# Performance work log

Hardware: AMD Instinct MI355X
Metric: run time of the kernel (lower is better)

## Reference

```python
import jax, jax.numpy as jnp
import numpy as np

DIM = 768
HEADS = 8
EPS = 1e-6


def _layernorm(x, gamma, beta):
    # torch: mean over last dim; std with Bessel correction (unbiased, ddof=1)
    mean = jnp.mean(x, axis=-1, keepdims=True)
    std = jnp.std(x, axis=-1, keepdims=True, ddof=1)
    return gamma * (x - mean) / (std + EPS) + beta


def setup_inputs() -> dict:
    key = jax.random.key(0)
    ks = jax.random.split(key, 8)
    s = 0.02
    return {
        "x": jax.random.normal(ks[0], (16384, DIM), dtype=jnp.float32),
        "wq_w": jax.random.normal(ks[1], (DIM, DIM), dtype=jnp.float32) * s,
        "wq_b": jnp.zeros((DIM,), dtype=jnp.float32),
        "wk_w": jax.random.normal(ks[2], (DIM, DIM), dtype=jnp.float32) * s,
        "wk_b": jnp.zeros((DIM,), dtype=jnp.float32),
        "wv_w": jax.random.normal(ks[3], (DIM, DIM), dtype=jnp.float32) * s,
        "wv_b": jnp.zeros((DIM,), dtype=jnp.float32),
        "d1_w": jax.random.normal(ks[4], (4 * DIM, DIM), dtype=jnp.float32) * s,
        "d1_b": jnp.zeros((4 * DIM,), dtype=jnp.float32),
        "d2_w": jax.random.normal(ks[5], (DIM, 4 * DIM), dtype=jnp.float32) * s,
        "d2_b": jnp.zeros((DIM,), dtype=jnp.float32),
        "g1": jnp.ones((1,), dtype=jnp.float32),
        "b1": jnp.zeros((1,), dtype=jnp.float32),
        "g2": jnp.ones((1,), dtype=jnp.float32),
        "b2": jnp.zeros((1,), dtype=jnp.float32),
    }


def reference(x, wq_w, wq_b, wk_w, wk_b, wv_w, wv_b,
              d1_w, d1_b, d2_w, d2_b, g1, b1, g2, b2):
    T = x.shape[0]
    # --- pre-LN + attention ---
    xn = _layernorm(x, g1, b1)                      # [T, D]
    q = xn @ wq_w.T + wq_b                          # [T, D]
    k = xn @ wk_w.T + wk_b
    v = xn @ wv_w.T + wv_b
    # faithful to q.view(-1, num_heads, key_dim): groups of HEADS tokens
    q = q.reshape(T // HEADS, HEADS, DIM)
    k = k.reshape(T // HEADS, HEADS, DIM)
    v = v.reshape(T // HEADS, HEADS, DIM)
    scores = jnp.einsum('ghd,gkd->ghk', q, k) / jnp.sqrt(jnp.float32(DIM))
    attn_w = jax.nn.softmax(scores, axis=-1)        # [T/8, 8, 8]
    attn = jnp.einsum('ghk,gkd->ghd', attn_w, v).reshape(T, DIM)
    x = attn + x
    # --- pre-LN + MLP ---
    xn = _layernorm(x, g2, b2)
    h = jax.nn.gelu(xn @ d1_w.T + d1_b, approximate=False)  # [T, 4D]
    x = (h @ d2_w.T + d2_b) + x
    return x
```

## Files before the change

kernel.cpp:

```cpp
#include <hip/hip_runtime.h>
#include <stdint.h>

#define DIM 768
#define HDIM 3072

typedef unsigned short u16;
typedef unsigned char u8;
typedef unsigned int u32;
typedef __bf16 bf16x8 __attribute__((ext_vector_type(8)));
typedef float f32x2 __attribute__((ext_vector_type(2)));
typedef float f32x4 __attribute__((ext_vector_type(4)));
typedef float f32x16 __attribute__((ext_vector_type(16)));
typedef int i32x8 __attribute__((ext_vector_type(8)));

__device__ __forceinline__ u16 f2b(float f) {
    union { float f; unsigned i; } v; v.f = f;
    unsigned r = (v.i + 0x7FFFu + ((v.i >> 16) & 1u)) >> 16;
    return (u16)r;
}
__device__ __forceinline__ unsigned pack2b(float a, float b) {
    return (unsigned)f2b(a) | ((unsigned)f2b(b) << 16);
}
__device__ __forceinline__ float gelu_f(float v) {
    float u = v * (1.5957691216f + 0.07135481627f * v * v);
    float e = __builtin_amdgcn_exp2f(-1.442695041f * u);
    return v * __builtin_amdgcn_rcpf(1.0f + e);
}
__device__ __forceinline__ void gl_lds16(const void* g, void* l) {
    __builtin_amdgcn_global_load_lds(
        (__attribute__((address_space(1))) void*)(g),
        (__attribute__((address_space(3))) void*)(l), 16, 0, 0);
}

__global__ __launch_bounds__(256) void cvt_all(
    const float4* __restrict__ wq, const float4* __restrict__ wk, const float4* __restrict__ wv,
    const float4* __restrict__ d1, const float4* __restrict__ d2,
    const float* __restrict__ bq, const float* __restrict__ bk, const float* __restrict__ bv,
    ushort4* __restrict__ o_d1, unsigned* __restrict__ o_d2,
    unsigned* __restrict__ o_qkv, float* __restrict__ o_bias) {
    const int i = blockIdx.x * 256 + threadIdx.x;
    const int y = blockIdx.y;
    if (y == 0) {
        float4 v = d1[i];
        ushort4 o;
        o.x = f2b(v.x); o.y = f2b(v.y); o.z = f2b(v.z); o.w = f2b(v.w);
        o_d1[i] = o;
    } else if (y == 1) {
        float4 v = d2[i];
        int p = __builtin_amdgcn_cvt_pk_fp8_f32(v.x * 32.f, v.y * 32.f, 0, false);
        p = __builtin_amdgcn_cvt_pk_fp8_f32(v.z * 32.f, v.w * 32.f, p, true);
        o_d2[i] = (unsigned)p;
    } else {
        if (i < 442368) {
            float4 v = (i < 147456) ? wq[i] : (i < 294912 ? wk[i - 147456] : wv[i - 294912]);
            int p = __builtin_amdgcn_cvt_pk_fp8_f32(v.x * 32.f, v.y * 32.f, 0, false);
            p = __builtin_amdgcn_cvt_pk_fp8_f32(v.z * 32.f, v.w * 32.f, p, true);
            o_qkv[i] = (unsigned)p;
        } else if (i < 442944) {
            const int j = (i - 442368) * 4;
#pragma unroll
            for (int e = 0; e < 4; ++e) {
                int f = j + e;
                float v = (f < 768) ? bq[f] : (f < 1536 ? bk[f - 768] : bv[f - 1536]);
                o_bias[f] = v;
            }
        }
    }
}

__global__ __launch_bounds__(256) void ln_rows_f8(const float* __restrict__ x, u8* __restrict__ xn,
                                                  const float* __restrict__ g, const float* __restrict__ b) {
    int row = blockIdx.x * 4 + (threadIdx.x >> 6);
    int lane = threadIdx.x & 63;
    const float* xr = x + (size_t)row * DIM + lane * 12;
    float v[12];
#pragma unroll
    for (int i = 0; i < 3; ++i) {
        float4 t = ((const float4*)xr)[i];
        v[i * 4 + 0] = t.x; v[i * 4 + 1] = t.y; v[i * 4 + 2] = t.z; v[i * 4 + 3] = t.w;
    }
    float s = 0.f, ss = 0.f;
#pragma unroll
    for (int i = 0; i < 12; ++i) { s += v[i]; ss += v[i] * v[i]; }
#pragma unroll
    for (int o = 32; o; o >>= 1) { s += __shfl_xor(s, o); ss += __shfl_xor(ss, o); }
    float mean = s * (1.f / DIM);
    float var = (ss - (float)DIM * mean * mean) * (1.f / (DIM - 1));
    float denom = sqrtf(var) + 1e-6f;
    float sc = g[0] / denom, bb = b[0] - mean * sc;
    unsigned* outp = (unsigned*)(xn + (size_t)row * DIM + lane * 12);
#pragma unroll
    for (int i = 0; i < 3; ++i) {
        int p = __builtin_amdgcn_cvt_pk_fp8_f32(v[i * 4 + 0] * sc + bb, v[i * 4 + 1] * sc + bb, 0, false);
        p = __builtin_amdgcn_cvt_pk_fp8_f32(v[i * 4 + 2] * sc + bb, v[i * 4 + 3] * sc + bb, p, true);
        outp[i] = (unsigned)p;
    }
}

template <int EPI, int N, int K>
__global__ __launch_bounds__(256)
void gemm_f8(const u8* __restrict__ A, const u8* __restrict__ B,
             const float* __restrict__ bias, const float* __restrict__ resid,
             u8* __restrict__ Co, float* __restrict__ Cf) {
    __shared__ __align__(16) u8 smem[32768];
    u8* As = smem;
    u8* Bs = smem + 16384;
    const int tid = threadIdx.x, lane = tid & 63, wave = tid >> 6;
    const int row0 = blockIdx.x * 128, col0 = blockIdx.y * 128;
    const int wm = (wave >> 1) * 64, wn = (wave & 1) * 64;
    f32x16 acc[2][2] = {};

    const int srow = lane >> 3;
    const int schunk = ((lane & 7) ^ srow) * 16;
    const u8* Ag = A + (size_t)(row0 + wave * 8 + srow) * K + schunk;
    const u8* Bg = B + (size_t)(col0 + wave * 8 + srow) * K + schunk;
    const size_t s32 = (size_t)32 * K;
    u8* AsW = As + wave * 1024;
    u8* BsW = Bs + wave * 1024;

    const int r31 = lane & 31, khalf = lane >> 5;

    for (int kb = 0; kb < K; kb += 128) {
#pragma unroll
        for (int i = 0; i < 4; ++i) {
            gl_lds16(Ag + i * s32, AsW + i * 4096);
            gl_lds16(Bg + i * s32, BsW + i * 4096);
        }
        Ag += 128; Bg += 128;
        __syncthreads();
#pragma unroll
        for (int ks = 0; ks < 2; ++ks) {
            const int c0 = ks * 4 + khalf * 2;
            union { i32x8 v; uint4 q[2]; } af[2], bfr[2];
#pragma unroll
            for (int ib = 0; ib < 2; ++ib) {
                const int r = wm + ib * 32 + r31;
                const u8* base = As + r * 128;
                const int x7 = (r & 7);
                af[ib].q[0] = *(const uint4*)(base + ((c0 ^ x7) * 16));
                af[ib].q[1] = *(const uint4*)(base + (((c0 + 1) ^ x7) * 16));
            }
#pragma unroll
            for (int jb = 0; jb < 2; ++jb) {
                const int r = wn + jb * 32 + r31;
                const u8* base = Bs + r * 128;
                const int x7 = (r & 7);
                bfr[jb].q[0] = *(const uint4*)(base + ((c0 ^ x7) * 16));
                bfr[jb].q[1] = *(const uint4*)(base + (((c0 + 1) ^ x7) * 16));
            }
#pragma unroll
            for (int ib = 0; ib < 2; ++ib)
#pragma unroll
                for (int jb = 0; jb < 2; ++jb)
                    acc[ib][jb] = __builtin_amdgcn_mfma_scale_f32_32x32x64_f8f6f4(
                        bfr[jb].v, af[ib].v, acc[ib][jb], 0, 0,
                        0, 0x7A7A7A7A,
                        0, 0x7F7F7F7F);
        }
        __syncthreads();
    }
    if (EPI == 0) {
        u32* Cs = (u32*)smem;
#pragma unroll
        for (int ib = 0; ib < 2; ++ib) {
            const int row = wm + ib * 32 + r31;
            const int rx = row & 31;
#pragma unroll
            for (int jb = 0; jb < 2; ++jb)
#pragma unroll
                for (int gq = 0; gq < 4; ++gq) {
                    const int cb = wn + jb * 32 + gq * 8 + 4 * khalf;
                    float4 bv = *(const float4*)(bias + col0 + cb);
                    float v0 = acc[ib][jb][gq * 4 + 0] + bv.x;
                    float v1 = acc[ib][jb][gq * 4 + 1] + bv.y;
                    float v2 = acc[ib][jb][gq * 4 + 2] + bv.z;
                    float v3 = acc[ib][jb][gq * 4 + 3] + bv.w;
                    int p = __builtin_amdgcn_cvt_pk_fp8_f32(v0, v1, 0, false);
                    p = __builtin_amdgcn_cvt_pk_fp8_f32(v2, v3, p, true);
                    Cs[row * 32 + ((cb >> 2) ^ rx)] = (u32)p;
                }
        }
        __syncthreads();
#pragma unroll
        for (int pr = 0; pr < 4; ++pr) {
            const int r = pr * 32 + (tid >> 3);
            const int rx = r & 31;
            const int dwb = (tid & 7) * 4;
            uint4 o;
            o.x = Cs[r * 32 + ((dwb + 0) ^ rx)];
            o.y = Cs[r * 32 + ((dwb + 1) ^ rx)];
            o.z = Cs[r * 32 + ((dwb + 2) ^ rx)];
            o.w = Cs[r * 32 + ((dwb + 3) ^ rx)];
            *(uint4*)(Co + (size_t)(row0 + r) * N + col0 + dwb * 4) = o;
        }
    } else {
        float* Cs = (float*)smem;
#pragma unroll
        for (int pass = 0; pass < 2; ++pass) {
            const int ss = (wm >> 1) + r31;
            const int sx = ss & 7;
#pragma unroll
            for (int jb = 0; jb < 2; ++jb)
#pragma unroll
                for (int gq = 0; gq < 4; ++gq) {
                    const int cb = wn + jb * 32 + gq * 8 + 4 * khalf;
                    float4 bv = *(const float4*)(bias + col0 + cb);
                    float4 v;
                    v.x = acc[pass][jb][gq * 4 + 0] + bv.x;
                    v.y = acc[pass][jb][gq * 4 + 1] + bv.y;
                    v.z = acc[pass][jb][gq * 4 + 2] + bv.z;
                    v.w = acc[pass][jb][gq * 4 + 3] + bv.w;
                    *(float4*)(Cs + ss * 128 + (((cb >> 2) ^ sx) << 2)) = v;
                }
            __syncthreads();
            const int s = tid >> 2;
            const int grow = row0 + (s >> 5) * 64 + pass * 32 + (s & 31);
#pragma unroll
            for (int k = 0; k < 8; ++k) {
                const int c = k * 4 + (tid & 3);
                float4 v = *(const float4*)(Cs + s * 128 + ((c ^ (s & 7)) << 2));
                const size_t gi = (size_t)grow * N + col0 + c * 4;
                float4 rv = *(const float4*)(resid + gi);
                v.x += rv.x; v.y += rv.y; v.z += rv.z; v.w += rv.w;
                *(float4*)(Cf + gi) = v;
            }
            if (pass == 0) __syncthreads();
        }
    }
}

template <int N, int K>
__global__ __launch_bounds__(256)
void gemm_up(const u16* __restrict__ A, const u16* __restrict__ B,
             const float* __restrict__ bias, u8* __restrict__ C8) {
    __shared__ __align__(16) u16 As[128 * 64];
    __shared__ __align__(16) u16 Bs[128 * 64];
    const int tid = threadIdx.x;
    const int row0 = blockIdx.x * 128, col0 = blockIdx.y * 128;
    const int lane = tid & 63, wave = tid >> 6;
    const int wm = (wave >> 1) * 64, wn = (wave & 1) * 64;
    const int r31 = lane & 31, khalf = lane >> 5;
    f32x16 acc[2][2] = {};

    const int srow = lane >> 3;
    const int schunk = (lane & 7) ^ srow;
    const u16* Ag = A + (size_t)(row0 + wave * 8 + srow) * K + schunk * 8;
    const u16* Bg = B + (size_t)(col0 + wave * 8 + srow) * K + schunk * 8;
    const size_t s32 = (size_t)32 * K;
    u16* AsW = &As[wave * 512];
    u16* BsW = &Bs[wave * 512];

    const int xr = r31 & 7;
    const u16* a0base = &As[(wm + r31) * 64];
    const u16* a1base = &As[(wm + 32 + r31) * 64];
    const u16* b0base = &Bs[(wn + r31) * 64];
    const u16* b1base = &Bs[(wn + 32 + r31) * 64];

    for (int kb = 0; kb < K; kb += 64) {
#pragma unroll
        for (int i = 0; i < 4; ++i) {
            gl_lds16(Ag + i * s32, AsW + i * 2048);
            gl_lds16(Bg + i * s32, BsW + i * 2048);
        }
        Ag += 64; Bg += 64;
        __syncthreads();
#pragma unroll
        for (int ks = 0; ks < 4; ++ks) {
            const int cp = ((ks * 2 + khalf) ^ xr) * 8;
            bf16x8 af0 = *(const bf16x8*)(a0base + cp);
            bf16x8 af1 = *(const bf16x8*)(a1base + cp);
            bf16x8 bf0 = *(const bf16x8*)(b0base + cp);
            bf16x8 bf1 = *(const bf16x8*)(b1base + cp);
            acc[0][0] = __builtin_amdgcn_mfma_f32_32x32x16_bf16(bf0, af0, acc[0][0], 0, 0, 0);
            acc[0][1] = __builtin_amdgcn_mfma_f32_32x32x16_bf16(bf1, af0, acc[0][1], 0, 0, 0);
            acc[1][0] = __builtin_amdgcn_mfma_f32_32x32x16_bf16(bf0, af1, acc[1][0], 0, 0, 0);
            acc[1][1] = __builtin_amdgcn_mfma_f32_32x32x16_bf16(bf1, af1, acc[1][1], 0, 0, 0);
        }
        __syncthreads();
    }
    u32* Cs = (u32*)As;
#pragma unroll
    for (int ib = 0; ib < 2; ++ib) {
        const int row = wm + ib * 32 + r31;
        const int rx = row & 31;
#pragma unroll
        for (int jb = 0; jb < 2; ++jb)
#pragma unroll
            for (int gq = 0; gq < 4; ++gq) {
                const int cb = wn + jb * 32 + gq * 8 + 4 * khalf;
                float4 bv = *(const float4*)(bias + col0 + cb);
                float v0 = gelu_f(acc[ib][jb][gq * 4 + 0] + bv.x);
                float v1 = gelu_f(acc[ib][jb][gq * 4 + 1] + bv.y);
                float v2 = gelu_f(acc[ib][jb][gq * 4 + 2] + bv.z);
                float v3 = gelu_f(acc[ib][jb][gq * 4 + 3] + bv.w);
                int p = __builtin_amdgcn_cvt_pk_fp8_f32(v0, v1, 0, false);
                p = __builtin_amdgcn_cvt_pk_fp8_f32(v2, v3, p, true);
                Cs[row * 32 + ((cb >> 2) ^ rx)] = (u32)p;
            }
    }
    __syncthreads();
#pragma unroll
    for (int pr = 0; pr < 4; ++pr) {
        const int r = pr * 32 + (tid >> 3);
        const int rx = r & 31;
        const int dwb = (tid & 7) * 4;
        uint4 o;
        o.x = Cs[r * 32 + ((dwb + 0) ^ rx)];
        o.y = Cs[r * 32 + ((dwb + 1) ^ rx)];
        o.z = Cs[r * 32 + ((dwb + 2) ^ rx)];
        o.w = Cs[r * 32 + ((dwb + 3) ^ rx)];
        *(uint4*)(C8 + (size_t)(row0 + r) * N + col0 + dwb * 4) = o;
    }
}

__global__ __launch_bounds__(256)
void attn_ln(const u8* __restrict__ qkv, const float* __restrict__ x,
             float* __restrict__ x1, u16* __restrict__ xn2,
             const float* __restrict__ g, const float* __restrict__ b) {
    __shared__ __align__(16) u8 sq[8 * 2304];
    __shared__ float sw[64];
    const int tid = threadIdx.x;
    const uint4* src = (const uint4*)(qkv + (size_t)blockIdx.x * (8 * 2304));
    uint4* dst = (uint4*)sq;
#pragma unroll
    for (int i = 0; i < 5; ++i) {
        int idx = tid + i * 256;
        if (idx < 1152) dst[idx] = src[idx];
    }
    __syncthreads();
    const u32* sq32 = (const u32*)sq;
    const int wave = tid >> 6, lane = tid & 63;
#pragma unroll 2
    for (int p = wave * 16; p < wave * 16 + 16; ++p) {
        const u32* qr = sq32 + (p >> 3) * 576 + lane * 3;
        const u32* kr = sq32 + (p & 7) * 576 + 192 + lane * 3;
        float s = 0.f;
#pragma unroll
        for (int i = 0; i < 3; ++i) {
            u32 qd = qr[i], kd = kr[i];
            f32x2 q0 = __builtin_amdgcn_cvt_pk_f32_fp8(qd, false);
            f32x2 q1 = __builtin_amdgcn_cvt_pk_f32_fp8(qd, true);
            f32x2 k0 = __builtin_amdgcn_cvt_pk_f32_fp8(kd, false);
            f32x2 k1 = __builtin_amdgcn_cvt_pk_f32_fp8(kd, true);
            s += q0[0] * k0[0] + q0[1] * k0[1] + q1[0] * k1[0] + q1[1] * k1[1];
        }
#pragma unroll
        for (int o = 32; o; o >>= 1) s += __shfl_xor(s, o);
        if (lane == 0) sw[p] = s;
    }
    __syncthreads();
    if (tid < 8) {
        const float scl = 0.03608439182435161f;
        float e[8]; float m = -1e30f;
#pragma unroll
        for (int j = 0; j < 8; ++j) m = fmaxf(m, sw[tid * 8 + j]);
        float sum = 0.f;
#pragma unroll
        for (int j = 0; j < 8; ++j) { e[j] = expf((sw[tid * 8 + j] - m) * scl); sum += e[j]; }
        float inv = 1.f / sum;
#pragma unroll
        for (int j = 0; j < 8; ++j) sw[tid * 8 + j] = e[j] * inv;
    }
    __syncthreads();
    const int h = tid >> 5, li = tid & 31;
    float w[8];
#pragma unroll
    for (int kk = 0; kk < 8; ++kk) w[kk] = sw[h * 8 + kk];
    const size_t trow = (size_t)blockIdx.x * 8 + h;
    const float* xr = x + trow * DIM;
    float* x1r = x1 + trow * DIM;
    float xv[24], s = 0.f, ss = 0.f;
#pragma unroll
    for (int wd = 0; wd < 3; ++wd) {
        const int d0 = wd * 256 + li * 8;
        float o[8] = {};
#pragma unroll
        for (int kk = 0; kk < 8; ++kk) {
            uint2 vv = *(const uint2*)(sq32 + kk * 576 + 384 + wd * 64 + li * 2);
            f32x2 a0 = __builtin_amdgcn_cvt_pk_f32_fp8(vv.x, false);
            f32x2 a1 = __builtin_amdgcn_cvt_pk_f32_fp8(vv.x, true);
            f32x2 a2 = __builtin_amdgcn_cvt_pk_f32_fp8(vv.y, false);
            f32x2 a3 = __builtin_amdgcn_cvt_pk_f32_fp8(vv.y, true);
            o[0] += w[kk] * a0[0]; o[1] += w[kk] * a0[1];
            o[2] += w[kk] * a1[0]; o[3] += w[kk] * a1[1];
            o[4] += w[kk] * a2[0]; o[5] += w[kk] * a2[1];
            o[6] += w[kk] * a3[0]; o[7] += w[kk] * a3[1];
        }
        float4 xa = *(const float4*)(xr + d0);
        float4 xb = *(const float4*)(xr + d0 + 4);
        float vals[8] = { o[0] + xa.x, o[1] + xa.y, o[2] + xa.z, o[3] + xa.w,
                          o[4] + xb.x, o[5] + xb.y, o[6] + xb.z, o[7] + xb.w };
        float4 w0, w1;
        w0.x = vals[0]; w0.y = vals[1]; w0.z = vals[2]; w0.w = vals[3];
        w1.x = vals[4]; w1.y = vals[5]; w1.z = vals[6]; w1.w = vals[7];
        *(float4*)(x1r + d0) = w0;
        *(float4*)(x1r + d0 + 4) = w1;
#pragma unroll
        for (int e = 0; e < 8; ++e) {
            xv[wd * 8 + e] = vals[e];
            s += vals[e]; ss += vals[e] * vals[e];
        }
    }
#pragma unroll
    for (int o2 = 16; o2; o2 >>= 1) { s += __shfl_xor(s, o2); ss += __shfl_xor(ss, o2); }
    float mean = s * (1.f / 768.f);
    float var = (ss - 768.f * mean * mean) * (1.f / 767.f);
    float denom = sqrtf(var) + 1e-6f;
    float sc = g[0] / denom, bb = b[0] - mean * sc;
    u16* xnr = xn2 + trow * DIM;
#pragma unroll
    for (int wd = 0; wd < 3; ++wd) {
        const int d0 = wd * 256 + li * 8;
        uint4 o;
        o.x = pack2b(xv[wd * 8 + 0] * sc + bb, xv[wd * 8 + 1] * sc + bb);
        o.y = pack2b(xv[wd * 8 + 2] * sc + bb, xv[wd * 8 + 3] * sc + bb);
        o.z = pack2b(xv[wd * 8 + 4] * sc + bb, xv[wd * 8 + 5] * sc + bb);
        o.w = pack2b(xv[wd * 8 + 6] * sc + bb, xv[wd * 8 + 7] * sc + bb);
        *(uint4*)(xnr + d0) = o;
    }
}

extern "C" void kernel_launch(void* const* d_in, const int* in_sizes, int n_in,
                              void* d_out, int out_size, void* d_ws, size_t ws_size,
                              hipStream_t stream) {
    (void)n_in; (void)out_size; (void)ws_size;
    const float* x    = (const float*)d_in[0];
    const float* wq_w = (const float*)d_in[1];
    const float* wq_b = (const float*)d_in[2];
    const float* wk_w = (const float*)d_in[3];
    const float* wk_b = (const float*)d_in[4];
    const float* wv_w = (const float*)d_in[5];
    const float* wv_b = (const float*)d_in[6];
    const float* d1_w = (const float*)d_in[7];
    const float* d1_b = (const float*)d_in[8];
    const float* d2_w = (const float*)d_in[9];
    const float* d2_b = (const float*)d_in[10];
    const float* g1 = (const float*)d_in[11];
    const float* b1 = (const float*)d_in[12];
    const float* g2 = (const float*)d_in[13];
    const float* b2 = (const float*)d_in[14];
    float* out = (float*)d_out;
    char* ws = (char*)d_ws;

    const int T = in_sizes[0] / DIM;

    u8*    w_qkv8 = (u8*)(ws);
    u16*   w_d1   = (u16*)(ws + 1769472);
    u8*    w_d28  = (u8*)(ws + 6488064);
    float* b_qkv  = (float*)(ws + 8847360);
    u16*   xn2    = (u16*)(ws + 8856576);
    float* x1     = (float*)(ws + 34022400);
    u8*    xn1_8  = (u8*)(ws + 34022400);
    u8*    qkv8   = (u8*)(ws + 84354048);
    u8*    h8     = (u8*)(ws + 84354048);

    cvt_all<<<dim3(2304, 3), 256, 0, stream>>>(
        (const float4*)wq_w, (const float4*)wk_w, (const float4*)wv_w,
        (const float4*)d1_w, (const float4*)d2_w,
        wq_b, wk_b, wv_b,
        (ushort4*)w_d1, (unsigned*)w_d28, (unsigned*)w_qkv8, b_qkv);

    ln_rows_f8<<<T / 4, 256, 0, stream>>>(x, xn1_8, g1, b1);
    gemm_f8<0, 2304, 768><<<dim3(T / 128, 18), 256, 0, stream>>>(xn1_8, w_qkv8, b_qkv, nullptr, qkv8, nullptr);
    attn_ln<<<T / 8, 256, 0, stream>>>(qkv8, x, x1, xn2, g2, b2);
    gemm_up<3072, 768><<<dim3(T / 128, 24), 256, 0, stream>>>(xn2, w_d1, d1_b, h8);
    gemm_f8<2, 768, 3072><<<dim3(T / 128, 6), 256, 0, stream>>>(h8, w_d28, d2_b, x1, nullptr, out);
}
```

Measured before the change: 353.5 us.

## Double-buffer LDS tiles in fp8 and bf16 GEMM kernels

Both GEMM kernels now keep two LDS stages and issue the global-to-LDS loads for tile t+1 before computing on tile t. This is meant to overlap memory latency with MFMA work instead of stalling on each tile load. LDS use doubles to 64KB per block, which may lower occupancy. The gemm_f8 loop body is only partly visible, so whether its end-of-iteration barrier stays correct cannot be confirmed.

```diff
diff --git a/kernel.cpp b/kernel.cpp
--- a/kernel.cpp
+++ b/kernel.cpp
@@ -102,9 +102,7 @@
 void gemm_f8(const u8* __restrict__ A, const u8* __restrict__ B,
              const float* __restrict__ bias, const float* __restrict__ resid,
              u8* __restrict__ Co, float* __restrict__ Cf) {
-    __shared__ __align__(16) u8 smem[32768];
-    u8* As = smem;
-    u8* Bs = smem + 16384;
+    __shared__ __align__(16) u8 smem[65536];
     const int tid = threadIdx.x, lane = tid & 63, wave = tid >> 6;
     const int row0 = blockIdx.x * 128, col0 = blockIdx.y * 128;
     const int wm = (wave >> 1) * 64, wn = (wave & 1) * 64;
@@ -115,19 +113,28 @@
     const u8* Ag = A + (size_t)(row0 + wave * 8 + srow) * K + schunk;
     const u8* Bg = B + (size_t)(col0 + wave * 8 + srow) * K + schunk;
     const size_t s32 = (size_t)32 * K;
-    u8* AsW = As + wave * 1024;
-    u8* BsW = Bs + wave * 1024;
-
+    const int woff = wave * 1024;
     const int r31 = lane & 31, khalf = lane >> 5;
-
-    for (int kb = 0; kb < K; kb += 128) {
+    constexpr int NT = K / 128;
+
+    auto STG = [&](int t) {
+        u8* As = smem + (t & 1) * 32768 + woff;
+        u8* Bs = smem + (t & 1) * 32768 + 16384 + woff;
+        const u8* ag = Ag + t * 128;
+        const u8* bg = Bg + t * 128;
 #pragma unroll
         for (int i = 0; i < 4; ++i) {
-            gl_lds16(Ag + i * s32, AsW + i * 4096);
-            gl_lds16(Bg + i * s32, BsW + i * 4096);
-        }
-        Ag += 128; Bg += 128;
-        __syncthreads();
+            gl_lds16(ag + i * s32, As + i * 4096);
+            gl_lds16(bg + i * s32, Bs + i * 4096);
+        }
+    };
+
+    STG(0);
+    __syncthreads();
+    for (int t = 0; t < NT; ++t) {
+        if (t + 1 < NT) STG(t + 1);
+        const u8* As = smem + (t & 1) * 32768;
+        const u8* Bs = As + 16384;
 #pragma unroll
         for (int ks = 0; ks < 2; ++ks) {
             const int c0 = ks * 4 + khalf * 2;
@@ -233,8 +240,7 @@
 __global__ __launch_bounds__(256)
 void gemm_up(const u16* __restrict__ A, const u16* __restrict__ B,
              const float* __restrict__ bias, u8* __restrict__ C8) {
-    __shared__ __align__(16) u16 As[128 * 64];
-    __shared__ __align__(16) u16 Bs[128 * 64];
+    __shared__ __align__(16) u16 AB[32768];
     const int tid = threadIdx.x;
     const int row0 = blockIdx.x * 128, col0 = blockIdx.y * 128;
     const int lane = tid & 63, wave = tid >> 6;
@@ -247,30 +253,37 @@
     const u16* Ag = A + (size_t)(row0 + wave * 8 + srow) * K + schunk * 8;
     const u16* Bg = B + (size_t)(col0 + wave * 8 + srow) * K + schunk * 8;
     const size_t s32 = (size_t)32 * K;
-    u16* AsW = &As[wave * 512];
-    u16* BsW = &Bs[wave * 512];
-
+    const int woff = wave * 512;
     const int xr = r31 & 7;
-    const u16* a0base = &As[(wm + r31) * 64];
-    const u16* a1base = &As[(wm + 32 + r31) * 64];
-    const u16* b0base = &Bs[(wn + r31) * 64];
-    const u16* b1base = &Bs[(wn + 32 + r31) * 64];
-
-    for (int kb = 0; kb < K; kb += 64) {
+    constexpr int NT = K / 64;
+
+    auto STG = [&](int t) {
+        u16* As = AB + (t & 1) * 16384 + woff;
+        u16* Bs = AB + (t & 1) * 16384 + 8192 + woff;
+        const u16* ag = Ag + t * 64;
+        const u16* bg = Bg + t * 64;
 #pragma unroll
         for (int i = 0; i < 4; ++i) {
-            gl_lds16(Ag + i * s32, AsW + i * 2048);
-            gl_lds16(Bg + i * s32, BsW + i * 2048);
-        }
-        Ag += 64; Bg += 64;
-        __syncthreads();
+            gl_lds16(ag + i * s32, As + i * 2048);
+            gl_lds16(bg + i * s32, Bs + i * 2048);
+        }
+    };
+
+    STG(0);
+    __syncthreads();
+    for (int t = 0; t < NT; ++t) {
+        if (t + 1 < NT) STG(t + 1);
+        const u16* As = AB + (t & 1) * 16384;
+        const u16* Bs = As + 8192;
+        const u16* a0base = As + (wm + r31) * 64;
+        const u16* b0base = Bs + (wn + r31) * 64;
 #pragma unroll
         for (int ks = 0; ks < 4; ++ks) {
             const int cp = ((ks * 2 + khalf) ^ xr) * 8;
             bf16x8 af0 = *(const bf16x8*)(a0base + cp);
-            bf16x8 af1 = *(const bf16x8*)(a1base + cp);
+            bf16x8 af1 = *(const bf16x8*)(a0base + 2048 + cp);
             bf16x8 bf0 = *(const bf16x8*)(b0base + cp);
-            bf16x8 bf1 = *(const bf16x8*)(b1base + cp);
+            bf16x8 bf1 = *(const bf16x8*)(b0base + 2048 + cp);
             acc[0][0] = __builtin_amdgcn_mfma_f32_32x32x16_bf16(bf0, af0, acc[0][0], 0, 0, 0);
             acc[0][1] = __builtin_amdgcn_mfma_f32_32x32x16_bf16(bf1, af0, acc[0][1], 0, 0, 0);
             acc[1][0] = __builtin_amdgcn_mfma_f32_32x32x16_bf16(bf0, af1, acc[1][0], 0, 0, 0);
@@ -278,7 +291,7 @@
         }
         __syncthreads();
     }
-    u32* Cs = (u32*)As;
+    u32* Cs = (u32*)AB;
 #pragma unroll
     for (int ib = 0; ib < 2; ++ib) {
         const int row = wm + ib * 32 + r31;
```

New measurement: 391.4 us. 1.11x slower.
